# Kernel tuning notes

Measured on AMD Instinct MI355X. Metric: run time of the kernel, lower is better.

## Reference

```python
import jax, jax.numpy as jnp
import numpy as np

N, E = 50000, 500000
D_NODE, D_EDGE, N_REL, N_CLS = 128, 128, 64, 16


def setup_inputs() -> dict:
    key = jax.random.key(0)
    ks = jax.random.split(key, 16)
    cat = 2 * D_NODE + D_EDGE  # 384
    s = 0.05
    return {
        "node_features": jax.random.normal(ks[0], (N, D_NODE), jnp.float32),
        "edge_features": jax.random.normal(ks[1], (E, D_EDGE), jnp.float32),
        "edge_index": jax.random.randint(ks[2], (2, E), 0, N, jnp.int32),
        "labels_for_rel_emb": jax.random.randint(ks[3], (E,), 0, N_REL, jnp.int32),
        "rel_emb": jax.random.normal(ks[4], (N_REL, D_EDGE), jnp.float32) * s,
        "msg_W": jax.random.normal(ks[5], (D_NODE, cat), jnp.float32) * s,
        "msg_b": jnp.zeros((D_NODE,), jnp.float32),
        "gru_w_ih": jax.random.normal(ks[6], (3 * D_NODE, D_NODE), jnp.float32) * s,
        "gru_w_hh": jax.random.normal(ks[7], (3 * D_NODE, D_NODE), jnp.float32) * s,
        "gru_b_ih": jnp.zeros((3 * D_NODE,), jnp.float32),
        "gru_b_hh": jnp.zeros((3 * D_NODE,), jnp.float32),
        "cls_W1": jax.random.normal(ks[8], (D_EDGE, cat), jnp.float32) * s,
        "cls_b1": jnp.zeros((D_EDGE,), jnp.float32),
        "cls_W2": jax.random.normal(ks[9], (N_CLS, D_EDGE), jnp.float32) * s,
        "cls_b2": jnp.zeros((N_CLS,), jnp.float32),
    }


def reference(node_features, edge_features, edge_index, labels_for_rel_emb,
              rel_emb, msg_W, msg_b, gru_w_ih, gru_w_hh, gru_b_ih, gru_b_hh,
              cls_W1, cls_b1, cls_W2, cls_b2):
    src, tgt = edge_index[0], edge_index[1]
    nf = node_features
    rel_feat = rel_emb[labels_for_rel_emb]                      # [E, d_edge]
    h = jnp.concatenate([nf[src], nf[tgt], rel_feat], axis=-1)  # [E, 384]
    msg = jax.nn.gelu(h @ msg_W.T + msg_b, approximate=False)   # [E, d_node]
    agg = jax.ops.segment_sum(msg, tgt, num_segments=nf.shape[0])  # [N, d_node]
    # torch.nn.GRUCell(agg, nf)
    gi = agg @ gru_w_ih.T + gru_b_ih
    gh = nf @ gru_w_hh.T + gru_b_hh
    i_r, i_z, i_n = jnp.split(gi, 3, axis=-1)
    h_r, h_z, h_n = jnp.split(gh, 3, axis=-1)
    r = jax.nn.sigmoid(i_r + h_r)
    z = jax.nn.sigmoid(i_z + h_z)
    n = jnp.tanh(i_n + r * h_n)
    nf_u = (1.0 - z) * n + z * nf
    c = jnp.concatenate([nf_u[src], nf_u[tgt], edge_features], axis=-1)  # [E, 384]
    hc = jax.nn.gelu(c @ cls_W1.T + cls_b1, approximate=False)           # [E, d_edge]
    return hc @ cls_W2.T + cls_b2                                        # [E, num_classes]
```

## Files before the change

kernel.cpp:

```cpp
#include <hip/hip_runtime.h>
#include <math.h>

#define N_NODES 50000
#define N_EDGES 500000
#define D 128
#define CAT 384

typedef __bf16 v8bf __attribute__((ext_vector_type(8)));
typedef __bf16 v2bf __attribute__((ext_vector_type(2)));
typedef float v4f __attribute__((ext_vector_type(4)));

__device__ __forceinline__ float erf_fast(float x) {
    float ax = fabsf(x);
    float t = __builtin_amdgcn_rcpf(fmaf(0.3275911f, ax, 1.0f));
    float p = fmaf(1.061405429f, t, -1.453152027f);
    p = fmaf(p, t, 1.421413741f);
    p = fmaf(p, t, -0.284496736f);
    p = fmaf(p, t, 0.254829592f);
    p = p * t;
    float e = __expf(-ax * ax);
    float r = 1.0f - p * e;
    return copysignf(r, x);
}

__device__ __forceinline__ float gelu_fast(float x) {
    return 0.5f * x * (1.0f + erf_fast(x * 0.70710678118654752440f));
}

__device__ __forceinline__ float sigmoid_fast(float x) {
    float e = __expf(-x);
    return __builtin_amdgcn_rcpf(1.0f + e);
}

__device__ __forceinline__ float tanh_fast(float x) {
    float e = __expf(2.0f * x);
    return 1.0f - 2.0f * __builtin_amdgcn_rcpf(e + 1.0f);
}

__device__ __forceinline__ v8bf cvt8(const float* __restrict__ p) {
    float4 f0 = *(const float4*)p;
    float4 f1 = *(const float4*)(p + 4);
    v8bf r;
    r[0] = (__bf16)f0.x; r[1] = (__bf16)f0.y; r[2] = (__bf16)f0.z; r[3] = (__bf16)f0.w;
    r[4] = (__bf16)f1.x; r[5] = (__bf16)f1.y; r[6] = (__bf16)f1.z; r[7] = (__bf16)f1.w;
    return r;
}

__global__ __launch_bounds__(256) void k_pre(const float* __restrict__ msgW,
                                             const float* __restrict__ W1,
                                             const float* __restrict__ W2,
                                             const float* __restrict__ wih,
                                             const float* __restrict__ whh,
                                             __bf16* __restrict__ WB,
                                             const float* __restrict__ rel_emb,
                                             const float* __restrict__ msg_b,
                                             __bf16* __restrict__ RPB,
                                             const int* __restrict__ ei,
                                             int* __restrict__ counts) {
    int bid = blockIdx.x;
    int t = threadIdx.x;
    if (bid < 712) {
        int i = bid * 256 + t;
        float v;
        if (i < 32768) {
            int j = i >> 7, k = i & 127;
            v = (j < 128) ? msgW[j * CAT + k] : msgW[(j - 128) * CAT + 128 + k];
        } else if (i < 65536) {
            int ii = i - 32768; int j = ii >> 7, k = ii & 127;
            v = (j < 128) ? W1[j * CAT + k] : W1[(j - 128) * CAT + 128 + k];
        } else if (i < 81920) {
            int ii = i - 65536; int j = ii >> 7, k = ii & 127;
            v = W1[j * CAT + 256 + k];
        } else if (i < 83968) {
            v = W2[i - 81920];
        } else if (i < 133120) {
            v = wih[i - 83968];
        } else {
            v = whh[i - 133120];
        }
        WB[i] = (__bf16)v;
    } else if (bid < 744) {
        int r = (bid - 712) * 2 + (t >> 7);
        int j = t & 127;
        const float* er = rel_emb + r * D;
        const float* wr = msgW + j * CAT + 2 * D;
        float acc = msg_b[j];
        #pragma unroll 8
        for (int k = 0; k < D; ++k) acc += er[k] * wr[k];
        RPB[r * D + j] = (__bf16)acc;
    } else {
        int e = (bid - 744) * 256 + t;
        if (e < N_EDGES) atomicAdd(&counts[ei[N_EDGES + e]], 1);
    }
}

__global__ __launch_bounds__(256) void k_proj2_f32(const float* __restrict__ in,
                                                   const __bf16* __restrict__ wb,
                                                   __bf16* __restrict__ out) {
    int t = threadIdx.x;
    int lane = t & 63, wid = t >> 6;
    int g = lane >> 4, c = lane & 15;
    int nbase = blockIdx.x * 64 + wid * 16;

    int nrow = min(nbase + c, N_NODES - 1);
    const float* ir = in + (size_t)nrow * D + g * 8;
    v8bf afrag[4];
    #pragma unroll
    for (int kc = 0; kc < 4; ++kc) afrag[kc] = cvt8(ir + kc * 32);

    #pragma unroll
    for (int half = 0; half < 2; ++half) {
        v4f acc[8];
        #pragma unroll 2
        for (int jt = 0; jt < 8; ++jt) {
            const __bf16* wr = wb + (size_t)(half * 128 + 8 * c + jt) * 128 + g * 8;
            v4f a4 = (v4f){0.f, 0.f, 0.f, 0.f};
            #pragma unroll
            for (int kc = 0; kc < 4; ++kc)
                a4 = __builtin_amdgcn_mfma_f32_16x16x32_bf16(afrag[kc], *(const v8bf*)(wr + kc * 32), a4, 0, 0, 0);
            acc[jt] = a4;
        }
        #pragma unroll
        for (int r = 0; r < 4; ++r) {
            int node = nbase + g * 4 + r;
            v8bf o;
            #pragma unroll
            for (int jt = 0; jt < 8; ++jt) o[jt] = (__bf16)acc[jt][r];
            if (node < N_NODES)
                *(v8bf*)(out + (size_t)node * 256 + half * 128 + 8 * c) = o;
        }
    }
}

__global__ __launch_bounds__(256) void k_proj2_b16(const __bf16* __restrict__ in,
                                                   const __bf16* __restrict__ wb,
                                                   __bf16* __restrict__ out) {
    int t = threadIdx.x;
    int lane = t & 63, wid = t >> 6;
    int g = lane >> 4, c = lane & 15;
    int nbase = blockIdx.x * 64 + wid * 16;

    int nrow = min(nbase + c, N_NODES - 1);
    const __bf16* ir = in + (size_t)nrow * D + g * 8;
    v8bf afrag[4];
    #pragma unroll
    for (int kc = 0; kc < 4; ++kc) afrag[kc] = *(const v8bf*)(ir + kc * 32);

    #pragma unroll
    for (int half = 0; half < 2; ++half) {
        v4f acc[8];
        #pragma unroll 2
        for (int jt = 0; jt < 8; ++jt) {
            const __bf16* wr = wb + (size_t)(half * 128 + 8 * c + jt) * 128 + g * 8;
            v4f a4 = (v4f){0.f, 0.f, 0.f, 0.f};
            #pragma unroll
            for (int kc = 0; kc < 4; ++kc)
                a4 = __builtin_amdgcn_mfma_f32_16x16x32_bf16(afrag[kc], *(const v8bf*)(wr + kc * 32), a4, 0, 0, 0);
            acc[jt] = a4;
        }
        #pragma unroll
        for (int r = 0; r < 4; ++r) {
            int node = nbase + g * 4 + r;
            v8bf o;
            #pragma unroll
            for (int jt = 0; jt < 8; ++jt) o[jt] = (__bf16)acc[jt][r];
            if (node < N_NODES)
                *(v8bf*)(out + (size_t)node * 256 + half * 128 + 8 * c) = o;
        }
    }
}

__global__ __launch_bounds__(256) void k_scan(const int* __restrict__ counts,
                                              int* __restrict__ offsets,
                                              int* __restrict__ cursor) {
    __shared__ int part[256];
    int t = threadIdx.x;
    const int CH = 196;
    int lo = t * CH, hi = min(lo + CH, N_NODES);
    int s = 0;
    for (int i = lo; i < hi; ++i) s += counts[i];
    part[t] = s;
    __syncthreads();
    for (int d = 1; d < 256; d <<= 1) {
        int v = (t >= d) ? part[t - d] : 0;
        __syncthreads();
        part[t] += v;
        __syncthreads();
    }
    int run = (t == 0) ? 0 : part[t - 1];
    for (int i = lo; i < hi; ++i) {
        offsets[i] = run;
        cursor[i] = run;
        run += counts[i];
    }
    if (t == 255) offsets[N_NODES] = run;
}

__global__ __launch_bounds__(256) void k_scatter(const int* __restrict__ ei,
                                                 int* __restrict__ cursor,
                                                 int* __restrict__ elist) {
    int e = blockIdx.x * 256 + threadIdx.x;
    if (e < N_EDGES) {
        int slot = atomicAdd(&cursor[ei[N_EDGES + e]], 1);
        elist[slot] = e;
    }
}

__global__ __launch_bounds__(256) void k_agg(const __bf16* __restrict__ PSTB,
                                             const __bf16* __restrict__ RPB,
                                             const int* __restrict__ ei,
                                             const int* __restrict__ lab,
                                             const int* __restrict__ offsets,
                                             const int* __restrict__ elist,
                                             __bf16* __restrict__ agg) {
    int t = threadIdx.x;
    int wid = t >> 6, lane = t & 63;
    int n = blockIdx.x * 4 + wid;
    if (n >= N_NODES) return;
    int beg = offsets[n], end = offsets[n + 1];

    v2bf ptv = *(const v2bf*)(PSTB + (size_t)n * 256 + 128 + lane * 2);
    float pt0 = (float)ptv[0], pt1 = (float)ptv[1];

    float a0 = 0.f, a1 = 0.f;
    v2bf ps0 = {}, rp0 = {};
    int s1 = 0, l1 = 0;
    if (beg < end) {
        int e = elist[beg]; int s = ei[e]; int l = lab[e];
        ps0 = *(const v2bf*)(PSTB + (size_t)s * 256 + lane * 2);
        rp0 = *(const v2bf*)(RPB + (size_t)l * D + lane * 2);
    }
    if (beg + 1 < end) {
        int e = elist[beg + 1]; s1 = ei[e]; l1 = lab[e];
    }
    for (int idx = beg; idx < end; ++idx) {
        v2bf ps = ps0, rp = rp0;
        if (idx + 1 < end) {
            ps0 = *(const v2bf*)(PSTB + (size_t)s1 * 256 + lane * 2);
            rp0 = *(const v2bf*)(RPB + (size_t)l1 * D + lane * 2);
        }
        if (idx + 2 < end) {
            int e = elist[idx + 2]; s1 = ei[e]; l1 = lab[e];
        }
        a0 += gelu_fast((float)ps[0] + pt0 + (float)rp[0]);
        a1 += gelu_fast((float)ps[1] + pt1 + (float)rp[1]);
    }
    v2bf o; o[0] = (__bf16)a0; o[1] = (__bf16)a1;
    *(v2bf*)(agg + (size_t)n * D + lane * 2) = o;
}

__global__ __launch_bounds__(256) void k_gru_mfma(const __bf16* __restrict__ agg,
                                                  const float* __restrict__ nf,
                                                  const __bf16* __restrict__ WIH,
                                                  const __bf16* __restrict__ WHH,
                                                  const float* __restrict__ b_ih,
                                                  const float* __restrict__ b_hh,
                                                  __bf16* __restrict__ nfu) {
    int t = threadIdx.x;
    int lane = t & 63, wid = t >> 6;
    int g = lane >> 4, c = lane & 15;
    int nbase = blockIdx.x * 64 + wid * 16;

    int nrow = min(nbase + c, N_NODES - 1);
    const __bf16* ar = agg + (size_t)nrow * D + g * 8;
    const float* hr = nf + (size_t)nrow * D + g * 8;
    v8bf afrag[4], hfrag[4];
    #pragma unroll
    for (int kc = 0; kc < 4; ++kc) {
        afrag[kc] = *(const v8bf*)(ar + kc * 32);
        hfrag[kc] = cvt8(hr + kc * 32);
    }

    float h8[4][8];
    #pragma unroll
    for (int r = 0; r < 4; ++r) {
        int node = min(nbase + g * 4 + r, N_NODES - 1);
        float4 f0 = *(const float4*)(nf + (size_t)node * D + 8 * c);
        float4 f1 = *(const float4*)(nf + (size_t)node * D + 8 * c + 4);
        h8[r][0]=f0.x; h8[r][1]=f0.y; h8[r][2]=f0.z; h8[r][3]=f0.w;
        h8[r][4]=f1.x; h8[r][5]=f1.y; h8[r][6]=f1.z; h8[r][7]=f1.w;
    }

    v8bf o[4];
    for (int jt = 0; jt < 8; ++jt) {
        int j = 8 * c + jt;
        const __bf16* wir = WIH + (size_t)j * 128 + g * 8;
        const __bf16* whr = WHH + (size_t)j * 128 + g * 8;
        v4f a_ir = (v4f){0.f,0.f,0.f,0.f}, a_iz = a_ir, a_in = a_ir;
        v4f a_hr = a_ir, a_hz = a_ir, a_hn = a_ir;
        #pragma unroll
        for (int kc = 0; kc < 4; ++kc) {
            a_ir = __builtin_amdgcn_mfma_f32_16x16x32_bf16(afrag[kc], *(const v8bf*)(wir + kc * 32), a_ir, 0, 0, 0);
            a_iz = __builtin_amdgcn_mfma_f32_16x16x32_bf16(afrag[kc], *(const v8bf*)(wir + 128 * 128 + kc * 32), a_iz, 0, 0, 0);
            a_in = __builtin_amdgcn_mfma_f32_16x16x32_bf16(afrag[kc], *(const v8bf*)(wir + 256 * 128 + kc * 32), a_in, 0, 0, 0);
            a_hr = __builtin_amdgcn_mfma_f32_16x16x32_bf16(hfrag[kc], *(const v8bf*)(whr + kc * 32), a_hr, 0, 0, 0);
            a_hz = __builtin_amdgcn_mfma_f32_16x16x32_bf16(hfrag[kc], *(const v8bf*)(whr + 128 * 128 + kc * 32), a_hz, 0, 0, 0);
            a_hn = __builtin_amdgcn_mfma_f32_16x16x32_bf16(hfrag[kc], *(const v8bf*)(whr + 256 * 128 + kc * 32), a_hn, 0, 0, 0);
        }
        float bir = b_ih[j], biz = b_ih[128 + j], bin = b_ih[256 + j];
        float bhr = b_hh[j], bhz = b_hh[128 + j], bhn = b_hh[256 + j];
        #pragma unroll
        for (int r = 0; r < 4; ++r) {
            float irv = a_ir[r] + bir, hrv = a_hr[r] + bhr;
            float izv = a_iz[r] + biz, hzv = a_hz[r] + bhz;
            float inv = a_in[r] + bin, hnv = a_hn[r] + bhn;
            float rg = sigmoid_fast(irv + hrv);
            float zg = sigmoid_fast(izv + hzv);
            float ng = tanh_fast(inv + rg * hnv);
            o[r][jt] = (__bf16)((1.f - zg) * ng + zg * h8[r][jt]);
        }
    }
    #pragma unroll
    for (int r = 0; r < 4; ++r) {
        int node = nbase + g * 4 + r;
        if (node < N_NODES) *(v8bf*)(nfu + (size_t)node * D + 8 * c) = o[r];
    }
}

__global__ __launch_bounds__(256) void k_cls_mfma(const float* __restrict__ ef,
                                                  const __bf16* __restrict__ QSTB,
                                                  const __bf16* __restrict__ V3,
                                                  const float* __restrict__ b1,
                                                  const __bf16* __restrict__ W2B,
                                                  const float* __restrict__ b2,
                                                  const int* __restrict__ ei,
                                                  float* __restrict__ out) {
    __shared__ __align__(16) __bf16 hc_s[64][128];
    int t = threadIdx.x;
    int lane = t & 63, w = t >> 6;
    int g = lane >> 4, c = lane & 15;
    int e0 = blockIdx.x * 64;
    int e_base = e0 + w * 16;

    int er = min(e_base + c, N_EDGES - 1);
    const float* efr = ef + (size_t)er * D + g * 8;
    float4 efraw[8];
    #pragma unroll
    for (int kc = 0; kc < 4; ++kc) {
        efraw[2 * kc]     = *(const float4*)(efr + kc * 32);
        efraw[2 * kc + 1] = *(const float4*)(efr + kc * 32 + 4);
    }

    int sr[4], tr[4];
    #pragma unroll
    for (int r = 0; r < 4; ++r) {
        int e = min(e_base + g * 4 + r, N_EDGES - 1);
        sr[r] = ei[e];
        tr[r] = ei[N_EDGES + e];
    }
    v8bf qsv[4], qtv[4];
    #pragma unroll
    for (int r = 0; r < 4; ++r) {
        qsv[r] = *(const v8bf*)(QSTB + (size_t)sr[r] * 256 + 8 * c);
        qtv[r] = *(const v8bf*)(QSTB + (size_t)tr[r] * 256 + 128 + 8 * c);
    }
    float4 b1a = *(const float4*)(b1 + 8 * c);
    float4 b1b = *(const float4*)(b1 + 8 * c + 4);
    float b1r[8] = {b1a.x, b1a.y, b1a.z, b1a.w, b1b.x, b1b.y, b1b.z, b1b.w};

    v8bf afrag[4];
    #pragma unroll
    for (int kc = 0; kc < 4; ++kc) {
        v8bf a;
        float4 f0 = efraw[2 * kc], f1 = efraw[2 * kc + 1];
        a[0] = (__bf16)f0.x; a[1] = (__bf16)f0.y; a[2] = (__bf16)f0.z; a[3] = (__bf16)f0.w;
        a[4] = (__bf16)f1.x; a[5] = (__bf16)f1.y; a[6] = (__bf16)f1.z; a[7] = (__bf16)f1.w;
        afrag[kc] = a;
    }

    v4f acc[8];
    #pragma unroll
    for (int jt = 0; jt < 8; ++jt) {
        const __bf16* wr = V3 + (size_t)(8 * c + jt) * 128 + g * 8;
        v4f a4 = (v4f){0.f, 0.f, 0.f, 0.f};
        #pragma unroll
        for (int kc = 0; kc < 4; ++kc)
            a4 = __builtin_amdgcn_mfma_f32_16x16x32_bf16(afrag[kc], *(const v8bf*)(wr + kc * 32), a4, 0, 0, 0);
        acc[jt] = a4;
    }

    #pragma unroll
    for (int r = 0; r < 4; ++r) {
        int el = w * 16 + g * 4 + r;
        v8bf o;
        #pragma unroll
        for (int jt = 0; jt < 8; ++jt) {
            float v = acc[jt][r] + (float)qsv[r][jt] + (float)qtv[r][jt] + b1r[jt];
            o[jt] = (__bf16)gelu_fast(v);
        }
        *(v8bf*)&hc_s[el][8 * (c ^ (el & 7))] = o;
    }

    v4f acc2 = (v4f){0.f, 0.f, 0.f, 0.f};
    int arow = w * 16 + c;
    #pragma unroll
    for (int kc = 0; kc < 4; ++kc) {
        int ch = g + 4 * kc;
        v8bf aa = *(const v8bf*)&hc_s[arow][8 * (ch ^ (c & 7))];
        v8bf bb = *(const v8bf*)(W2B + c * 128 + ch * 8);
        acc2 = __builtin_amdgcn_mfma_f32_16x16x32_bf16(aa, bb, acc2, 0, 0, 0);
    }
    float b2c = b2[c];
    #pragma unroll
    for (int r = 0; r < 4; ++r) {
        int e = e_base + g * 4 + r;
        if (e < N_EDGES) out[(size_t)e * 16 + c] = acc2[r] + b2c;
    }
}

extern "C" void kernel_launch(void* const* d_in, const int* in_sizes, int n_in,
                              void* d_out, int out_size, void* d_ws, size_t ws_size,
                              hipStream_t stream) {
    const float* nf   = (const float*)d_in[0];
    const float* ef   = (const float*)d_in[1];
    const int*   ei   = (const int*)d_in[2];
    const int*   lab  = (const int*)d_in[3];
    const float* rel  = (const float*)d_in[4];
    const float* msgW = (const float*)d_in[5];
    const float* msgb = (const float*)d_in[6];
    const float* wih  = (const float*)d_in[7];
    const float* whh  = (const float*)d_in[8];
    const float* bih  = (const float*)d_in[9];
    const float* bhh  = (const float*)d_in[10];
    const float* W1   = (const float*)d_in[11];
    const float* b1   = (const float*)d_in[12];
    const float* W2   = (const float*)d_in[13];
    const float* b2   = (const float*)d_in[14];
    float* out = (float*)d_out;

    char* ws = (char*)d_ws;
    __bf16* WB      = (__bf16*)(ws);
    __bf16* RPB     = (__bf16*)(ws + 524288);
    int*    offsets = (int*)(ws + 1048576);
    int*    counts  = (int*)(ws + 1310720);
    int*    cursor  = (int*)(ws + 1572864);
    int*    elist   = (int*)(ws + 1835008);
    __bf16* PSTB    = (__bf16*)(ws + 4194304);
    __bf16* AGG     = (__bf16*)(ws + 33554432);
    __bf16* NFUB    = (__bf16*)(ws + 50331648);
    __bf16* QSTB    = PSTB;

    __bf16* WP1 = WB;
    __bf16* WQ1 = WB + 32768;
    __bf16* V3  = WB + 65536;
    __bf16* W2B = WB + 81920;
    __bf16* WIH = WB + 83968;
    __bf16* WHH = WB + 133120;

    int nblk = (N_NODES + 63) / 64;
    int eblk = (N_EDGES + 255) / 256;

    hipMemsetAsync(counts, 0, N_NODES * sizeof(int), stream);
    k_pre<<<744 + eblk, 256, 0, stream>>>(msgW, W1, W2, wih, whh, WB,
                                          rel, msgb, RPB, ei, counts);
    k_proj2_f32<<<nblk, 256, 0, stream>>>(nf, WP1, PSTB);
    k_scan<<<1, 256, 0, stream>>>(counts, offsets, cursor);
    k_scatter<<<eblk, 256, 0, stream>>>(ei, cursor, elist);
    k_agg<<<(N_NODES + 3) / 4, 256, 0, stream>>>(PSTB, RPB, ei, lab, offsets, elist, AGG);
    k_gru_mfma<<<nblk, 256, 0, stream>>>(AGG, nf, WIH, WHH, bih, bhh, NFUB);
    k_proj2_b16<<<nblk, 256, 0, stream>>>(NFUB, WQ1, QSTB);
    k_cls_mfma<<<(N_EDGES + 63) / 64, 256, 0, stream>>>(ef, QSTB, V3, b1, W2B, b2, ei, out);
}
```

Before: 590.8 us.

## Widen scan block, double-unroll aggregation prefetch, stage classifier weights in LDS

```diff
diff --git a/kernel.cpp b/kernel.cpp
--- a/kernel.cpp
+++ b/kernel.cpp
@@ -170,18 +170,18 @@
     }
 }
 
-__global__ __launch_bounds__(256) void k_scan(const int* __restrict__ counts,
-                                              int* __restrict__ offsets,
-                                              int* __restrict__ cursor) {
-    __shared__ int part[256];
-    int t = threadIdx.x;
-    const int CH = 196;
+__global__ __launch_bounds__(1024) void k_scan(const int* __restrict__ counts,
+                                               int* __restrict__ offsets,
+                                               int* __restrict__ cursor) {
+    __shared__ int part[1024];
+    int t = threadIdx.x;
+    const int CH = 49;
     int lo = t * CH, hi = min(lo + CH, N_NODES);
     int s = 0;
     for (int i = lo; i < hi; ++i) s += counts[i];
     part[t] = s;
     __syncthreads();
-    for (int d = 1; d < 256; d <<= 1) {
+    for (int d = 1; d < 1024; d <<= 1) {
         int v = (t >= d) ? part[t - d] : 0;
         __syncthreads();
         part[t] += v;
@@ -193,7 +193,7 @@
         cursor[i] = run;
         run += counts[i];
     }
-    if (t == 255) offsets[N_NODES] = run;
+    if (t == 1023) offsets[N_NODES] = run;
 }
 
 __global__ __launch_bounds__(256) void k_scatter(const int* __restrict__ ei,
@@ -223,27 +223,39 @@
     float pt0 = (float)ptv[0], pt1 = (float)ptv[1];
 
     float a0 = 0.f, a1 = 0.f;
-    v2bf ps0 = {}, rp0 = {};
-    int s1 = 0, l1 = 0;
     if (beg < end) {
-        int e = elist[beg]; int s = ei[e]; int l = lab[e];
-        ps0 = *(const v2bf*)(PSTB + (size_t)s * 256 + lane * 2);
-        rp0 = *(const v2bf*)(RPB + (size_t)l * D + lane * 2);
-    }
-    if (beg + 1 < end) {
-        int e = elist[beg + 1]; s1 = ei[e]; l1 = lab[e];
-    }
-    for (int idx = beg; idx < end; ++idx) {
-        v2bf ps = ps0, rp = rp0;
-        if (idx + 1 < end) {
-            ps0 = *(const v2bf*)(PSTB + (size_t)s1 * 256 + lane * 2);
-            rp0 = *(const v2bf*)(RPB + (size_t)l1 * D + lane * 2);
-        }
-        if (idx + 2 < end) {
-            int e = elist[idx + 2]; s1 = ei[e]; l1 = lab[e];
-        }
-        a0 += gelu_fast((float)ps[0] + pt0 + (float)rp[0]);
-        a1 += gelu_fast((float)ps[1] + pt1 + (float)rp[1]);
+        int mx = end - 1;
+        int eA = elist[beg];
+        int eB = elist[min(beg + 1, mx)];
+        int e2 = elist[min(beg + 2, mx)];
+        int e3 = elist[min(beg + 3, mx)];
+        int sA = ei[eA], lA = lab[eA];
+        int sB = ei[eB], lB = lab[eB];
+        int s2 = ei[e2], l2 = lab[e2];
+        int s3 = ei[e3], l3 = lab[e3];
+        v2bf psA = *(const v2bf*)(PSTB + (size_t)sA * 256 + lane * 2);
+        v2bf rpA = *(const v2bf*)(RPB + (size_t)lA * D + lane * 2);
+        v2bf psB = *(const v2bf*)(PSTB + (size_t)sB * 256 + lane * 2);
+        v2bf rpB = *(const v2bf*)(RPB + (size_t)lB * D + lane * 2);
+
+        for (int idx = beg; idx < end; idx += 2) {
+            v2bf cpsA = psA, crpA = rpA, cpsB = psB, crpB = rpB;
+            bool hasB = (idx + 1 < end);
+            psA = *(const v2bf*)(PSTB + (size_t)s2 * 256 + lane * 2);
+            rpA = *(const v2bf*)(RPB + (size_t)l2 * D + lane * 2);
+            psB = *(const v2bf*)(PSTB + (size_t)s3 * 256 + lane * 2);
+            rpB = *(const v2bf*)(RPB + (size_t)l3 * D + lane * 2);
+            int e4 = elist[min(idx + 4, mx)];
+            int e5 = elist[min(idx + 5, mx)];
+            s2 = ei[e4]; l2 = lab[e4];
+            s3 = ei[e5]; l3 = lab[e5];
+            a0 += gelu_fast((float)cpsA[0] + pt0 + (float)crpA[0]);
+            a1 += gelu_fast((float)cpsA[1] + pt1 + (float)crpA[1]);
+            if (hasB) {
+                a0 += gelu_fast((float)cpsB[0] + pt0 + (float)crpB[0]);
+                a1 += gelu_fast((float)cpsB[1] + pt1 + (float)crpB[1]);
+            }
+        }
     }
     v2bf o; o[0] = (__bf16)a0; o[1] = (__bf16)a1;
     *(v2bf*)(agg + (size_t)n * D + lane * 2) = o;
@@ -325,6 +337,7 @@
                                                   const float* __restrict__ b2,
                                                   const int* __restrict__ ei,
                                                   float* __restrict__ out) {
+    __shared__ __align__(16) __bf16 v3_s[128][128];
     __shared__ __align__(16) __bf16 hc_s[64][128];
     int t = threadIdx.x;
     int lane = t & 63, w = t >> 6;
@@ -348,6 +361,16 @@
         sr[r] = ei[e];
         tr[r] = ei[N_EDGES + e];
     }
+
+    #pragma unroll
+    for (int i = 0; i < 8; ++i) {
+        int idx = t * 8 + i;
+        int row = idx >> 4, ch = idx & 15;
+        v8bf v = *(const v8bf*)(V3 + row * 128 + ch * 8);
+        *(v8bf*)&v3_s[row][8 * (ch ^ ((row >> 3) & 7))] = v;
+    }
+    __syncthreads();
+
     v8bf qsv[4], qtv[4];
     #pragma unroll
     for (int r = 0; r < 4; ++r) {
@@ -371,11 +394,13 @@
     v4f acc[8];
     #pragma unroll
     for (int jt = 0; jt < 8; ++jt) {
-        const __bf16* wr = V3 + (size_t)(8 * c + jt) * 128 + g * 8;
+        int row = 8 * c + jt;
         v4f a4 = (v4f){0.f, 0.f, 0.f, 0.f};
         #pragma unroll
-        for (int kc = 0; kc < 4; ++kc)
-            a4 = __builtin_amdgcn_mfma_f32_16x16x32_bf16(afrag[kc], *(const v8bf*)(wr + kc * 32), a4, 0, 0, 0);
+        for (int kc = 0; kc < 4; ++kc) {
+            v8bf bb = *(const v8bf*)&v3_s[row][8 * ((g + 4 * kc) ^ (c & 7))];
+            a4 = __builtin_amdgcn_mfma_f32_16x16x32_bf16(afrag[kc], bb, a4, 0, 0, 0);
+        }
         acc[jt] = a4;
     }
 
@@ -454,7 +479,7 @@
     k_pre<<<744 + eblk, 256, 0, stream>>>(msgW, W1, W2, wih, whh, WB,
                                           rel, msgb, RPB, ei, counts);
     k_proj2_f32<<<nblk, 256, 0, stream>>>(nf, WP1, PSTB);
-    k_scan<<<1, 256, 0, stream>>>(counts, offsets, cursor);
+    k_scan<<<1, 1024, 0, stream>>>(counts, offsets, cursor);
     k_scatter<<<eblk, 256, 0, stream>>>(ei, cursor, elist);
     k_agg<<<(N_NODES + 3) / 4, 256, 0, stream>>>(PSTB, RPB, ei, lab, offsets, elist, AGG);
     k_gru_mfma<<<nblk, 256, 0, stream>>>(AGG, nf, WIH, WHH, bih, bhh, NFUB);
```

Result: faster. 515.2 us (-12.8%).
